# Performance work log

Hardware: AMD Instinct MI355X
Metric: run time of the kernel (lower is better)

## Reference

```python
import jax, jax.numpy as jnp
import numpy as np

N = 50000      # nodes
E = 800000     # edges (avg degree 16)
D = 64         # emb_dim
L = 5          # num_layer
BN_EPS = 1e-5


def setup_inputs() -> dict:
    key = jax.random.key(0)
    ks = jax.random.split(key, 10)
    x = jax.random.randint(ks[0], (N,), 0, 1)                      # indices into 1-row embedding
    edge_index = jax.random.randint(ks[1], (2, E), 0, N)
    edge_attr = jax.random.normal(ks[2], (E, 7), dtype=jnp.float32)
    s = lambda k, shape: (jax.random.normal(k, shape, dtype=jnp.float32) * 0.05)
    node_emb = s(ks[3], (1, D))
    # per-layer GINConv params, stacked on a leading layer axis for lax.scan
    We = s(ks[4], (L, 7, D));   be = jnp.zeros((L, D), jnp.float32)      # edge_encoder
    eps = jnp.zeros((L,), jnp.float32)                                   # GIN eps
    W1 = s(ks[5], (L, D, 2 * D)); b1 = jnp.zeros((L, 2 * D), jnp.float32)  # mlp linear1
    g1 = jnp.ones((L, 2 * D), jnp.float32); bb1 = jnp.zeros((L, 2 * D), jnp.float32)  # mlp BN
    W2 = s(ks[6], (L, 2 * D, D)); b2 = jnp.zeros((L, D), jnp.float32)    # mlp linear2
    g2 = jnp.ones((L, D), jnp.float32); bb2 = jnp.zeros((L, D), jnp.float32)  # outer BN
    return dict(x=x, edge_index=edge_index, edge_attr=edge_attr, node_emb=node_emb,
                We=We, be=be, eps=eps, W1=W1, b1=b1, g1=g1, bb1=bb1,
                W2=W2, b2=b2, g2=g2, bb2=bb2)


def _bn(a, g, b):
    # BatchNorm1d in training mode: batch statistics over node axis, biased var
    m = a.mean(axis=0)
    v = jnp.var(a, axis=0)
    return (a - m) * jax.lax.rsqrt(v + BN_EPS) * g + b


def reference(x, edge_index, edge_attr, node_emb, We, be, eps,
              W1, b1, g1, bb1, W2, b2, g2, bb2):
    src, dst = edge_index[0], edge_index[1]
    h = node_emb[x]                                    # [N, D]
    relu_flags = jnp.arange(L) < (L - 1)               # ReLU on all but last layer

    def step(h, p):
        We_, be_, eps_, W1_, b1_, g1_, bb1_, W2_, b2_, g2_, bb2_, flag = p
        ee = edge_attr @ We_ + be_                     # [E, D] edge embeddings
        msg = jax.nn.relu(h[src] + ee)                 # gather + elementwise
        agg = jax.ops.segment_sum(msg, dst, num_segments=N)  # scatter-add
        z = (1.0 + eps_) * h + agg                     # GIN combine
        a = jax.nn.relu(_bn(z @ W1_ + b1_, g1_, bb1_)) # mlp: lin -> BN -> ReLU
        hb = _bn(a @ W2_ + b2_, g2_, bb2_)             # lin -> outer BN
        h_new = jnp.where(flag, jax.nn.relu(hb), hb)   # dropout omitted (eval)
        return h_new, None

    h, _ = jax.lax.scan(step, h, (We, be, eps, W1, b1, g1, bb1, W2, b2, g2, bb2, relu_flags))
    return h                                           # JK='last'
```

## Files before the change

### kernel.cpp

```cpp
#include <hip/hip_runtime.h>
#include <hip/hip_fp16.h>

#define NN 50000
#define EE 800000
#define NB 782
#define NBKT 196
#define BCAP 4608

typedef _Float16 f16x8 __attribute__((ext_vector_type(8)));
typedef _Float16 f16x2 __attribute__((ext_vector_type(2)));
typedef float f32x4 __attribute__((ext_vector_type(4)));

__device__ __forceinline__ unsigned h2u(__half2 h) {
    union { __half2 h; unsigned u; } c; c.h = h; return c.u;
}
__device__ __forceinline__ f16x2 u2h(unsigned u) {
    union { unsigned u; f16x2 h; } c; c.u = u; return c.h;
}

__global__ __launch_bounds__(256) void bin_kernel(
    const int* __restrict__ ei, const float* __restrict__ ea,
    int* __restrict__ bktcur, int4* __restrict__ srec,
    unsigned short* __restrict__ sdst)
{
    __shared__ int cnt[NBKT], base[NBKT];
    const int t = threadIdx.x;
    if (t < NBKT) cnt[t] = 0;
    __syncthreads();
    const int e0 = blockIdx.x << 12;
    int meta[16];
#pragma unroll
    for (int j = 0; j < 16; ++j) {
        const int e = e0 + (j << 8) + t;
        if (e < EE) {
            const int d = ei[EE + e];
            const int bk = d >> 8;
            const int rk = atomicAdd(&cnt[bk], 1);
            meta[j] = (rk << 16) | (bk << 8) | (d & 255);
        } else meta[j] = -1;
    }
    __syncthreads();
    if (t < NBKT) base[t] = cnt[t] ? atomicAdd(&bktcur[t], cnt[t]) : 0;
    __syncthreads();
#pragma unroll
    for (int j = 0; j < 16; ++j) {
        if (meta[j] < 0) continue;
        const int bk = (meta[j] >> 8) & 255;
        const int slot = base[bk] + (meta[j] >> 16);
        if (slot >= BCAP) continue;
        const int pos = bk * BCAP + slot;
        const int e = e0 + (j << 8) + t;
        const int src = ei[e];
        const float* a = ea + e * 7;
        const unsigned h0 = __half_as_ushort(__float2half(a[0]));
        const unsigned h1 = __half_as_ushort(__float2half(a[1]));
        const unsigned h2 = __half_as_ushort(__float2half(a[2]));
        const unsigned h3 = __half_as_ushort(__float2half(a[3]));
        const unsigned h4 = __half_as_ushort(__float2half(a[4]));
        const unsigned h5 = __half_as_ushort(__float2half(a[5]));
        const unsigned h6 = __half_as_ushort(__float2half(a[6]));
        srec[pos] = make_int4((int)(h0 | (h1 << 16)), (int)(h2 | (h3 << 16)),
                              (int)(h4 | (h5 << 16)), (int)(h6 | ((unsigned)src << 16)));
        sdst[pos] = (unsigned short)(meta[j] & 255);
    }
}

__global__ __launch_bounds__(256) void bcountA_kernel(
    const int* __restrict__ bktcur, const unsigned short* __restrict__ sdst,
    int* __restrict__ deg, int* __restrict__ bsum)
{
    __shared__ int nc[256], sm[256];
    const int b = blockIdx.x, t = threadIdx.x;
    nc[t] = 0;
    __syncthreads();
    const int nE = min(bktcur[b], BCAP);
    const int sb = b * BCAP;
    for (int i = t; i < nE; i += 256) atomicAdd(&nc[(int)sdst[sb + i]], 1);
    __syncthreads();
    const int node = (b << 8) + t;
    if (node < NN) deg[node] = nc[t];
    sm[t] = (node < NN) ? ((nc[t] + 7) & ~7) : 0;
    __syncthreads();
    for (int o = 128; o > 0; o >>= 1) {
        if (t < o) sm[t] += sm[t + o];
        __syncthreads();
    }
    if (t == 0) bsum[b] = sm[0];
}

__global__ __launch_bounds__(256) void scanB_kernel(int* __restrict__ bsum) {
    __shared__ int sm[256];
    const int t = threadIdx.x;
    const int v = (t < 196) ? bsum[t] : 0;
    sm[t] = v;
    __syncthreads();
    for (int o = 1; o < 256; o <<= 1) {
        const int u = (t >= o) ? sm[t - o] : 0;
        __syncthreads();
        sm[t] += u;
        __syncthreads();
    }
    bsum[t] = sm[t] - v;
}

__global__ __launch_bounds__(256) void scanC_kernel(const int* __restrict__ deg,
                                                    const int* __restrict__ bsum,
                                                    int* __restrict__ off) {
    __shared__ int sm[256];
    const int t = threadIdx.x;
    const int i = (blockIdx.x << 8) + t;
    const int v = (i < NN) ? ((deg[i] + 7) & ~7) : 0;
    sm[t] = v;
    __syncthreads();
    for (int o = 1; o < 256; o <<= 1) {
        const int u = (t >= o) ? sm[t - o] : 0;
        __syncthreads();
        sm[t] += u;
        __syncthreads();
    }
    const int excl = bsum[blockIdx.x] + sm[t] - v;
    if (i < NN) off[i] = excl;
    else if (i == NN) off[NN] = excl;
}

__global__ __launch_bounds__(256) void place2_kernel(
    const int* __restrict__ bktcur, const int* __restrict__ off,
    const int4* __restrict__ srec, const unsigned short* __restrict__ sdst,
    int4* __restrict__ pea)
{
    __shared__ int curs[256];
    const int b = blockIdx.x, t = threadIdx.x;
    const int node = (b << 8) + t;
    curs[t] = (node < NN) ? off[node] : 0;
    __syncthreads();
    const int nE = min(bktcur[b], BCAP);
    const int sb = b * BCAP;
    for (int i = t; i < nE; i += 256) {
        const int ln = (int)sdst[sb + i];
        const int p = atomicAdd(&curs[ln], 1);
        pea[p] = srec[sb + i];
    }
    __syncthreads();
    if (node < NN) {
        const int end = off[node + 1];
        for (int p = curs[t]; p < end; ++p)
            pea[p] = make_int4(0, 0, 0, (int)(((unsigned)NN) << 16));
    }
}

__global__ __launch_bounds__(256) void wprep_kernel(
    const float* __restrict__ W1, const float* __restrict__ W2,
    const float* __restrict__ We, const float* __restrict__ be,
    _Float16* __restrict__ W1s, _Float16* __restrict__ W2s,
    unsigned* __restrict__ Wepk, unsigned* __restrict__ be2)
{
    const int i = (blockIdx.x << 8) + threadIdx.x;
    if (i < 40960) {
        const int l = i >> 13, j = i & 8191, k = j >> 7, n = j & 127;
        W1s[(l << 13) + ((((k >> 3) << 7) + n) << 3) + (k & 7)] = (_Float16)W1[i];
    } else if (i < 81920) {
        const int i2 = i - 40960;
        const int l = i2 >> 13, j = i2 & 8191, k = j >> 6, n = j & 63;
        W2s[(l << 13) + ((((k >> 3) << 6) + n) << 3) + (k & 7)] = (_Float16)W2[i2];
    } else if (i < 83040) {
        const int i3 = i - 81920;
        const int l = i3 / 224;
        const int r = i3 - l * 224;
        const int k = r >> 5, s = r & 31;
        const float* W = We + l * 448 + (k << 6) + (s << 1);
        Wepk[i3] = h2u(__floats2half2_rn(W[0], W[1]));
    } else if (i < 83200) {
        const int i4 = i - 83040;
        const int l = i4 >> 5, s = i4 & 31;
        const float* B = be + (l << 6) + (s << 1);
        be2[i4] = h2u(__floats2half2_rn(B[0], B[1]));
    }
}

__global__ __launch_bounds__(256) void hprep_kernel(
    const float* __restrict__ y2, const float* __restrict__ acc2,
    const float* __restrict__ g2p, const float* __restrict__ bb2p,
    __half* __restrict__ h16)
{
    __shared__ float scshL[128];
    const int t = threadIdx.x;
    if (t < 64) {
        float ss = 0.f, qq = 0.f;
#pragma unroll
        for (int c = 0; c < 8; ++c) {
            ss += acc2[(c << 7) + t];
            qq += acc2[(c << 7) + 64 + t];
        }
        const float m = ss * (1.0f / NN);
        const float v = fmaxf(qq * (1.0f / NN) - m * m, 0.0f);
        const float sc = g2p[t] * rsqrtf(v + 1e-5f);
        scshL[t] = sc;
        scshL[64 + t] = bb2p[t] - m * sc;
    }
    __syncthreads();
    const int i4 = (blockIdx.x << 8) + t;
    const float4 v = ((const float4*)y2)[i4];
    const int d0 = (i4 << 2) & 63;
    const float a = fmaxf(fmaf(v.x, scshL[d0 + 0], scshL[64 + d0 + 0]), 0.f);
    const float b = fmaxf(fmaf(v.y, scshL[d0 + 1], scshL[64 + d0 + 1]), 0.f);
    const float c = fmaxf(fmaf(v.z, scshL[d0 + 2], scshL[64 + d0 + 2]), 0.f);
    const float d = fmaxf(fmaf(v.w, scshL[d0 + 3], scshL[64 + d0 + 3]), 0.f);
    *(int2*)(h16 + (i4 << 2)) =
        make_int2((int)h2u(__floats2half2_rn(a, b)),
                  (int)h2u(__floats2half2_rn(c, d)));
}

__global__ __launch_bounds__(256) void hprep0_kernel(
    const int* __restrict__ x, const float* __restrict__ nemb,
    __half* __restrict__ h16, unsigned* __restrict__ z32)
{
    const int i4 = (blockIdx.x << 8) + threadIdx.x;
    if (blockIdx.x == 0 && threadIdx.x < 32)
        ((unsigned*)h16)[(NN << 5) + threadIdx.x] = 0xFBFFFBFFu;
    if (i4 < 1536) z32[1600000 + i4] = 0u;
    const int n = i4 >> 4;
    const float4 v = ((const float4*)nemb)[(x[n] << 4) + (i4 & 15)];
    *(int2*)(h16 + (i4 << 2)) =
        make_int2((int)h2u(__floats2half2_rn(v.x, v.y)),
                  (int)h2u(__floats2half2_rn(v.z, v.w)));
}

__global__ __launch_bounds__(256) void gather_kernel(
    const int* __restrict__ off, const int4* __restrict__ pea,
    const unsigned* __restrict__ h32,
    const unsigned* __restrict__ Wepk, const unsigned* __restrict__ be2,
    const float* __restrict__ epsp,
    unsigned* __restrict__ z32)
{
    const int t = threadIdx.x;
    const int lane = t & 63;
    const int s = lane & 31;
    const int n = (blockIdx.x << 3) + ((t >> 6) << 1) + (lane >> 5);

    const f16x2 w0 = u2h(Wepk[s]),       w1 = u2h(Wepk[32 + s]),
                w2 = u2h(Wepk[64 + s]),  w3 = u2h(Wepk[96 + s]),
                w4 = u2h(Wepk[128 + s]), w5 = u2h(Wepk[160 + s]),
                w6 = u2h(Wepk[192 + s]);
    const f16x2 beh = u2h(be2[s]);

    const int e0 = off[n], e1 = off[n + 1];

    f16x2 acc2 = (f16x2){(_Float16)0.f, (_Float16)0.f};
    int e = e0;
    if (((e1 - e0) >> 3) & 1) {
        int4 pk[8];
#pragma unroll
        for (int j = 0; j < 8; ++j) pk[j] = pea[e + j];
        unsigned hv[8];
#pragma unroll
        for (int j = 0; j < 8; ++j)
            hv[j] = h32[(((int)(((unsigned)pk[j].w) >> 16)) << 5) + s];
#pragma unroll
        for (int j = 0; j < 8; ++j) {
            const f16x2 a01 = u2h((unsigned)pk[j].x);
            const f16x2 a23 = u2h((unsigned)pk[j].y);
            const f16x2 a45 = u2h((unsigned)pk[j].z);
            const f16x2 a6x = u2h((unsigned)pk[j].w);
            f16x2 ee = beh;
            ee += (f16x2){a01[0], a01[0]} * w0;
            ee += (f16x2){a01[1], a01[1]} * w1;
            ee += (f16x2){a23[0], a23[0]} * w2;
            ee += (f16x2){a23[1], a23[1]} * w3;
            ee += (f16x2){a45[0], a45[0]} * w4;
            ee += (f16x2){a45[1], a45[1]} * w5;
            ee += (f16x2){a6x[0], a6x[0]} * w6;
            f16x2 m2 = u2h(hv[j]) + ee;
            const _Float16 zz = (_Float16)0.f;
            m2 = (f16x2){ m2[0] > zz ? m2[0] : zz, m2[1] > zz ? m2[1] : zz };
            acc2 += m2;
        }
        e += 8;
    }
    for (; e < e1; e += 16) {
        int4 pk[16];
#pragma unroll
        for (int j = 0; j < 16; ++j) pk[j] = pea[e + j];
        unsigned hv[16];
#pragma unroll
        for (int j = 0; j < 16; ++j)
            hv[j] = h32[(((int)(((unsigned)pk[j].w) >> 16)) << 5) + s];
#pragma unroll
        for (int j = 0; j < 16; ++j) {
            const f16x2 a01 = u2h((unsigned)pk[j].x);
            const f16x2 a23 = u2h((unsigned)pk[j].y);
            const f16x2 a45 = u2h((unsigned)pk[j].z);
            const f16x2 a6x = u2h((unsigned)pk[j].w);
            f16x2 ee = beh;
            ee += (f16x2){a01[0], a01[0]} * w0;
            ee += (f16x2){a01[1], a01[1]} * w1;
            ee += (f16x2){a23[0], a23[0]} * w2;
            ee += (f16x2){a23[1], a23[1]} * w3;
            ee += (f16x2){a45[0], a45[0]} * w4;
            ee += (f16x2){a45[1], a45[1]} * w5;
            ee += (f16x2){a6x[0], a6x[0]} * w6;
            f16x2 m2 = u2h(hv[j]) + ee;
            const _Float16 zz = (_Float16)0.f;
            m2 = (f16x2){ m2[0] > zz ? m2[0] : zz, m2[1] > zz ? m2[1] : zz };
            acc2 += m2;
        }
    }
    const f16x2 hn2 = u2h(h32[(n << 5) + s]);
    const float e1f = 1.0f + epsp[0];
    const float zLo = fmaf(e1f, (float)hn2[0], (float)acc2[0]);
    const float zHi = fmaf(e1f, (float)hn2[1], (float)acc2[1]);
    z32[(n << 5) + s] = h2u(__floats2half2_rn(zLo, zHi));
}

__global__ __launch_bounds__(256) void mm1_kernel(
    const _Float16* __restrict__ z16, const _Float16* __restrict__ W1s,
    const float* __restrict__ b1p, _Float16* __restrict__ y1h,
    float* __restrict__ acc1)
{
    __shared__ float smS[4][128], smQ[4][128];
    const int t = threadIdx.x;
    const int wv = t >> 6, lane = t & 63;
    const int q = lane >> 4, ln = lane & 15;
    const int r0 = blockIdx.x << 6;

    const int rowm = r0 + (wv << 4) + ln;
    const f16x8 af0 = *(const f16x8*)(z16 + rowm * 64 + (q << 3));
    const f16x8 af1 = *(const f16x8*)(z16 + rowm * 64 + 32 + (q << 3));

    f32x4 acc[8];
#pragma unroll
    for (int n0 = 0; n0 < 8; ++n0) acc[n0] = (f32x4){0.f, 0.f, 0.f, 0.f};
#pragma unroll
    for (int n0 = 0; n0 < 8; ++n0) {
        const f16x8 bf0 = *(const f16x8*)(W1s + (((q << 7) + (n0 << 4) + ln) << 3));
        const f16x8 bf1 = *(const f16x8*)(W1s + ((((4 + q) << 7) + (n0 << 4) + ln) << 3));
        acc[n0] = __builtin_amdgcn_mfma_f32_16x16x32_f16(af0, bf0, acc[n0], 0, 0, 0);
        acc[n0] = __builtin_amdgcn_mfma_f32_16x16x32_f16(af1, bf1, acc[n0], 0, 0, 0);
    }

    const int baseRow = r0 + (wv << 4) + (q << 2);
#pragma unroll
    for (int n0 = 0; n0 < 8; ++n0) {
        const int col = (n0 << 4) + ln;
        const float bb = b1p[col];
        float s = 0.f, sq = 0.f;
#pragma unroll
        for (int rg = 0; rg < 4; ++rg) {
            const int row = baseRow + rg;
            const float y = acc[n0][rg] + bb;
            y1h[row * 128 + col] = (_Float16)y;
            const float m = (row < NN) ? 1.f : 0.f;
            s = fmaf(m, y, s); sq = fmaf(m, y * y, sq);
        }
        s += __shfl_xor(s, 16); s += __shfl_xor(s, 32);
        sq += __shfl_xor(sq, 16); sq += __shfl_xor(sq, 32);
        if (lane < 16) { smS[wv][col] = s; smQ[wv][col] = sq; }
    }
    __syncthreads();
    if (t < 128) {
        const float s4 = smS[0][t] + smS[1][t] + smS[2][t] + smS[3][t];
        const float q4 = smQ[0][t] + smQ[1][t] + smQ[2][t] + smQ[3][t];
        float* a1 = acc1 + ((blockIdx.x & 7) << 8);
        atomicAdd(&a1[t], s4);
        atomicAdd(&a1[128 + t], q4);
    }
}

__global__ __launch_bounds__(256) void mm2_kernel(
    const _Float16* __restrict__ y1h, const float* __restrict__ acc1,
    const float* __restrict__ g1p, const float* __restrict__ bb1p,
    const _Float16* __restrict__ W2s, const float* __restrict__ b2,
    float* __restrict__ y2, float* __restrict__ acc2)
{
    __shared__ float smS[4][64], smQ[4][64];
    __shared__ float scshL[256];
    const int t = threadIdx.x;
    const int wv = t >> 6, lane = t & 63;
    const int q = lane >> 4, ln = lane & 15;
    const int r0 = blockIdx.x << 6;

    if (t < 128) {
        float ss = 0.f, qq = 0.f;
#pragma unroll
        for (int c = 0; c < 8; ++c) {
            ss += acc1[(c << 8) + t];
            qq += acc1[(c << 8) + 128 + t];
        }
        const float m = ss * (1.0f / NN);
        const float v = fmaxf(qq * (1.0f / NN) - m * m, 0.0f);
        const float sc = g1p[t] * rsqrtf(v + 1e-5f);
        scshL[t] = sc;
        scshL[128 + t] = bb1p[t] - m * sc;
    }
    __syncthreads();

    const int rowm = r0 + (wv << 4) + ln;
    f16x8 af[4];
#pragma unroll
    for (int ks = 0; ks < 4; ++ks) {
        const int k0 = (ks << 5) + (q << 3);
        const f16x8 raw = *(const f16x8*)(y1h + rowm * 128 + k0);
        f16x8 a;
#pragma unroll
        for (int j = 0; j < 8; ++j) {
            const float sc = scshL[k0 + j], sh = scshL[128 + k0 + j];
            a[j] = (_Float16)fmaxf(fmaf((float)raw[j], sc, sh), 0.f);
        }
        af[ks] = a;
    }

    f32x4 acc[4];
#pragma unroll
    for (int n0 = 0; n0 < 4; ++n0) acc[n0] = (f32x4){0.f, 0.f, 0.f, 0.f};
#pragma unroll
    for (int n0 = 0; n0 < 4; ++n0) {
#pragma unroll
        for (int ks = 0; ks < 4; ++ks) {
            const f16x8 bf = *(const f16x8*)(
                W2s + (((((ks << 2) + q) << 6) + (n0 << 4) + ln) << 3));
            acc[n0] = __builtin_amdgcn_mfma_f32_16x16x32_f16(af[ks], bf, acc[n0], 0, 0, 0);
        }
    }

    const int baseRow = r0 + (wv << 4) + (q << 2);
#pragma unroll
    for (int n0 = 0; n0 < 4; ++n0) {
        const int col = (n0 << 4) + ln;
        const float bb = b2[col];
        float s = 0.f, sq = 0.f;
#pragma unroll
        for (int rg = 0; rg < 4; ++rg) {
            const int row = baseRow + rg;
            const float y = acc[n0][rg] + bb;
            y2[row * 64 + col] = y;
            const float m = (row < NN) ? 1.f : 0.f;
            s = fmaf(m, y, s); sq = fmaf(m, y * y, sq);
        }
        s += __shfl_xor(s, 16); s += __shfl_xor(s, 32);
        sq += __shfl_xor(sq, 16); sq += __shfl_xor(sq, 32);
        if (lane < 16) { smS[wv][col] = s; smQ[wv][col] = sq; }
    }
    __syncthreads();
    if (t < 64) {
        const float s4 = smS[0][t] + smS[1][t] + smS[2][t] + smS[3][t];
        const float q4 = smQ[0][t] + smQ[1][t] + smQ[2][t] + smQ[3][t];
        float* a2 = acc2 + ((blockIdx.x & 7) << 7);
        atomicAdd(&a2[t], s4);
        atomicAdd(&a2[64 + t], q4);
    }
}

__global__ __launch_bounds__(256) void final_kernel(
    const float* __restrict__ y2, const float* __restrict__ acc2,
    const float* __restrict__ g2p, const float* __restrict__ bb2p,
    float* __restrict__ out)
{
    __shared__ float scshL[128];
    const int t = threadIdx.x;
    if (t < 64) {
        float ss = 0.f, qq = 0.f;
#pragma unroll
        for (int c = 0; c < 8; ++c) {
            ss += acc2[(c << 7) + t];
            qq += acc2[(c << 7) + 64 + t];
        }
        const float m = ss * (1.0f / NN);
        const float v = fmaxf(qq * (1.0f / NN) - m * m, 0.0f);
        const float sc = g2p[t] * rsqrtf(v + 1e-5f);
        scshL[t] = sc;
        scshL[64 + t] = bb2p[t] - m * sc;
    }
    __syncthreads();
    const int i4 = (blockIdx.x << 8) + t;
    const float4 v = ((const float4*)y2)[i4];
    const int d0 = (i4 << 2) & 63;
    float4 o;
    o.x = fmaf(v.x, scshL[d0 + 0], scshL[64 + d0 + 0]);
    o.y = fmaf(v.y, scshL[d0 + 1], scshL[64 + d0 + 1]);
    o.z = fmaf(v.z, scshL[d0 + 2], scshL[64 + d0 + 2]);
    o.w = fmaf(v.w, scshL[d0 + 3], scshL[64 + d0 + 3]);
    ((float4*)out)[i4] = o;
}

extern "C" void kernel_launch(void* const* d_in, const int* in_sizes, int n_in,
                              void* d_out, int out_size, void* d_ws, size_t ws_size,
                              hipStream_t stream)
{
    const int*   x    = (const int*)d_in[0];
    const int*   ei   = (const int*)d_in[1];
    const float* ea   = (const float*)d_in[2];
    const float* nemb = (const float*)d_in[3];
    const float* We   = (const float*)d_in[4];
    const float* be   = (const float*)d_in[5];
    const float* eps  = (const float*)d_in[6];
    const float* W1   = (const float*)d_in[7];
    const float* b1   = (const float*)d_in[8];
    const float* g1   = (const float*)d_in[9];
    const float* bb1  = (const float*)d_in[10];
    const float* W2   = (const float*)d_in[11];
    const float* b2   = (const float*)d_in[12];
    const float* g2   = (const float*)d_in[13];
    const float* bb2  = (const float*)d_in[14];
    float* out = (float*)d_out;

    int*      iws   = (int*)d_ws;
    float*    fws   = (float*)d_ws;
    int*      off   = iws + 0;
    int*      deg   = iws + 50048;
    int*      bsum  = iws + 150144;
    int*      bktcur= iws + 150784;
    float*    accbuf= fws + 151040;
    _Float16* W1s   = (_Float16*)(fws + 451072);
    _Float16* W2s   = (_Float16*)(fws + 471552);
    unsigned* Wepk  = (unsigned*)(fws + 492032);
    unsigned* be2   = (unsigned*)(fws + 493152);
    int4*     pea   = (int4*)(iws + 493312);
    _Float16* z16   = (_Float16*)(fws + 5093312);
    _Float16* y1h   = (_Float16*)(fws + 6694848);
    float*    y2    = fws + 6694848;
    __half*   h16   = (__half*)(fws + 9897920);

    int4*           srec = (int4*)(fws + 5093312);
    unsigned short* sdst = (unsigned short*)(fws + 9897920);

    hipMemsetAsync(bktcur, 0, (166400 - 150784) * sizeof(int), stream);

    bin_kernel    <<<196,  256, 0, stream>>>(ei, ea, bktcur, srec, sdst);
    bcountA_kernel<<<NBKT, 256, 0, stream>>>(bktcur, sdst, deg, bsum);
    scanB_kernel  <<<1,    256, 0, stream>>>(bsum);
    scanC_kernel  <<<196,  256, 0, stream>>>(deg, bsum, off);
    place2_kernel <<<NBKT, 256, 0, stream>>>(bktcur, off, srec, sdst, pea);
    wprep_kernel  <<<325,  256, 0, stream>>>(W1, W2, We, be, W1s, W2s, Wepk, be2);
    hprep0_kernel <<<3125, 256, 0, stream>>>(x, nemb, h16, (unsigned*)z16);

    for (int l = 0; l < 5; ++l) {
        float* acc1 = accbuf + l * 3072;
        float* acc2 = accbuf + l * 3072 + 2048;

        gather_kernel<<<6250, 256, 0, stream>>>(
            off, pea, (const unsigned*)h16, Wepk + l * 224, be2 + l * 32,
            eps + l, (unsigned*)z16);

        mm1_kernel<<<NB, 256, 0, stream>>>(z16, W1s + l * 8192, b1 + l * 128,
                                           y1h, acc1);

        mm2_kernel<<<NB, 256, 0, stream>>>(y1h, acc1, g1 + l * 128, bb1 + l * 128,
                                           W2s + l * 8192, b2 + l * 64, y2, acc2);

        if (l < 4)
            hprep_kernel<<<3125, 256, 0, stream>>>(y2, acc2, g2 + l * 64,
                                                   bb2 + l * 64, h16);
    }

    final_kernel<<<3125, 256, 0, stream>>>(y2, accbuf + 4 * 3072 + 2048,
                                           g2 + 4 * 64, bb2 + 4 * 64, out);
}
```

Measured before the change: 417.5 us.

## Fuse CSR build into per-bucket kernel with fixed slots and merge prep kernels

Replaces the count/scan/scan/place chain with one kernel per bucket. Each bucket computes a local prefix sum and writes its edges into a fixed-capacity slot region, and start/end pairs replace the global offset array. The weight-prep and initial-h kernels are merged into one launch. This removes four launches and the global scan passes, but adds padding gaps in the edge array and assumes each bucket's padded edge count fits its fixed slot.

```diff
diff --git a/kernel.cpp b/kernel.cpp
--- a/kernel.cpp
+++ b/kernel.cpp
@@ -6,6 +6,7 @@
 #define NB 782
 #define NBKT 196
 #define BCAP 4608
+#define PSLOT 6144
 
 typedef _Float16 f16x8 __attribute__((ext_vector_type(8)));
 typedef _Float16 f16x2 __attribute__((ext_vector_type(2)));
@@ -65,11 +66,12 @@
     }
 }
 
-__global__ __launch_bounds__(256) void bcountA_kernel(
-    const int* __restrict__ bktcur, const unsigned short* __restrict__ sdst,
-    int* __restrict__ deg, int* __restrict__ bsum)
-{
-    __shared__ int nc[256], sm[256];
+__global__ __launch_bounds__(256) void buildB_kernel(
+    const int* __restrict__ bktcur, const int4* __restrict__ srec,
+    const unsigned short* __restrict__ sdst,
+    int2* __restrict__ offSE, int4* __restrict__ pea)
+{
+    __shared__ int nc[256], sm[256], curs[256];
     const int b = blockIdx.x, t = threadIdx.x;
     nc[t] = 0;
     __syncthreads();
@@ -78,21 +80,9 @@
     for (int i = t; i < nE; i += 256) atomicAdd(&nc[(int)sdst[sb + i]], 1);
     __syncthreads();
     const int node = (b << 8) + t;
-    if (node < NN) deg[node] = nc[t];
-    sm[t] = (node < NN) ? ((nc[t] + 7) & ~7) : 0;
-    __syncthreads();
-    for (int o = 128; o > 0; o >>= 1) {
-        if (t < o) sm[t] += sm[t + o];
-        __syncthreads();
-    }
-    if (t == 0) bsum[b] = sm[0];
-}
-
-__global__ __launch_bounds__(256) void scanB_kernel(int* __restrict__ bsum) {
-    __shared__ int sm[256];
-    const int t = threadIdx.x;
-    const int v = (t < 196) ? bsum[t] : 0;
-    sm[t] = v;
+    const int used = nc[t];
+    const int pd = (node < NN) ? ((used + 7) & ~7) : 0;
+    sm[t] = pd;
     __syncthreads();
     for (int o = 1; o < 256; o <<= 1) {
         const int u = (t >= o) ? sm[t - o] : 0;
@@ -100,41 +90,10 @@
         sm[t] += u;
         __syncthreads();
     }
-    bsum[t] = sm[t] - v;
-}
-
-__global__ __launch_bounds__(256) void scanC_kernel(const int* __restrict__ deg,
-                                                    const int* __restrict__ bsum,
-                                                    int* __restrict__ off) {
-    __shared__ int sm[256];
-    const int t = threadIdx.x;
-    const int i = (blockIdx.x << 8) + t;
-    const int v = (i < NN) ? ((deg[i] + 7) & ~7) : 0;
-    sm[t] = v;
-    __syncthreads();
-    for (int o = 1; o < 256; o <<= 1) {
-        const int u = (t >= o) ? sm[t - o] : 0;
-        __syncthreads();
-        sm[t] += u;
-        __syncthreads();
-    }
-    const int excl = bsum[blockIdx.x] + sm[t] - v;
-    if (i < NN) off[i] = excl;
-    else if (i == NN) off[NN] = excl;
-}
-
-__global__ __launch_bounds__(256) void place2_kernel(
-    const int* __restrict__ bktcur, const int* __restrict__ off,
-    const int4* __restrict__ srec, const unsigned short* __restrict__ sdst,
-    int4* __restrict__ pea)
-{
-    __shared__ int curs[256];
-    const int b = blockIdx.x, t = threadIdx.x;
-    const int node = (b << 8) + t;
-    curs[t] = (node < NN) ? off[node] : 0;
-    __syncthreads();
-    const int nE = min(bktcur[b], BCAP);
-    const int sb = b * BCAP;
+    const int st = b * PSLOT + sm[t] - pd;
+    if (node < NN) offSE[node] = make_int2(st, st + pd);
+    curs[t] = st;
+    __syncthreads();
     for (int i = t; i < nE; i += 256) {
         const int ln = (int)sdst[sb + i];
         const int p = atomicAdd(&curs[ln], 1);
@@ -142,19 +101,33 @@
     }
     __syncthreads();
     if (node < NN) {
-        const int end = off[node + 1];
+        const int end = st + pd;
         for (int p = curs[t]; p < end; ++p)
             pea[p] = make_int4(0, 0, 0, (int)(((unsigned)NN) << 16));
     }
 }
 
-__global__ __launch_bounds__(256) void wprep_kernel(
+__global__ __launch_bounds__(256) void prep_kernel(
+    const int* __restrict__ x, const float* __restrict__ nemb,
+    __half* __restrict__ h16, unsigned* __restrict__ z32,
     const float* __restrict__ W1, const float* __restrict__ W2,
     const float* __restrict__ We, const float* __restrict__ be,
     _Float16* __restrict__ W1s, _Float16* __restrict__ W2s,
     unsigned* __restrict__ Wepk, unsigned* __restrict__ be2)
 {
-    const int i = (blockIdx.x << 8) + threadIdx.x;
+    if (blockIdx.x < 3125) {
+        const int i4 = (blockIdx.x << 8) + threadIdx.x;
+        if (blockIdx.x == 0 && threadIdx.x < 32)
+            ((unsigned*)h16)[(NN << 5) + threadIdx.x] = 0xFBFFFBFFu;
+        if (i4 < 1536) z32[1600000 + i4] = 0u;
+        const int n = i4 >> 4;
+        const float4 v = ((const float4*)nemb)[(x[n] << 4) + (i4 & 15)];
+        *(int2*)(h16 + (i4 << 2)) =
+            make_int2((int)h2u(__floats2half2_rn(v.x, v.y)),
+                      (int)h2u(__floats2half2_rn(v.z, v.w)));
+        return;
+    }
+    const int i = ((blockIdx.x - 3125) << 8) + threadIdx.x;
     if (i < 40960) {
         const int l = i >> 13, j = i & 8191, k = j >> 7, n = j & 127;
         W1s[(l << 13) + ((((k >> 3) << 7) + n) << 3) + (k & 7)] = (_Float16)W1[i];
@@ -210,23 +183,8 @@
                   (int)h2u(__floats2half2_rn(c, d)));
 }
 
-__global__ __launch_bounds__(256) void hprep0_kernel(
-    const int* __restrict__ x, const float* __restrict__ nemb,
-    __half* __restrict__ h16, unsigned* __restrict__ z32)
-{
-    const int i4 = (blockIdx.x << 8) + threadIdx.x;
-    if (blockIdx.x == 0 && threadIdx.x < 32)
-        ((unsigned*)h16)[(NN << 5) + threadIdx.x] = 0xFBFFFBFFu;
-    if (i4 < 1536) z32[1600000 + i4] = 0u;
-    const int n = i4 >> 4;
-    const float4 v = ((const float4*)nemb)[(x[n] << 4) + (i4 & 15)];
-    *(int2*)(h16 + (i4 << 2)) =
-        make_int2((int)h2u(__floats2half2_rn(v.x, v.y)),
-                  (int)h2u(__floats2half2_rn(v.z, v.w)));
-}
-
 __global__ __launch_bounds__(256) void gather_kernel(
-    const int* __restrict__ off, const int4* __restrict__ pea,
+    const int2* __restrict__ offSE, const int4* __restrict__ pea,
     const unsigned* __restrict__ h32,
     const unsigned* __restrict__ Wepk, const unsigned* __restrict__ be2,
     const float* __restrict__ epsp,
@@ -243,7 +201,8 @@
                 w6 = u2h(Wepk[192 + s]);
     const f16x2 beh = u2h(be2[s]);
 
-    const int e0 = off[n], e1 = off[n + 1];
+    const int2 se = offSE[n];
+    const int e0 = se.x, e1 = se.y;
 
     f16x2 acc2 = (f16x2){(_Float16)0.f, (_Float16)0.f};
     int e = e0;
@@ -426,18 +385,18 @@
     for (int n0 = 0; n0 < 4; ++n0) {
         const int col = (n0 << 4) + ln;
         const float bb = b2[col];
-        float s = 0.f, sq = 0.f;
+        float sa = 0.f, sq = 0.f;
 #pragma unroll
         for (int rg = 0; rg < 4; ++rg) {
             const int row = baseRow + rg;
             const float y = acc[n0][rg] + bb;
             y2[row * 64 + col] = y;
             const float m = (row < NN) ? 1.f : 0.f;
-            s = fmaf(m, y, s); sq = fmaf(m, y * y, sq);
-        }
-        s += __shfl_xor(s, 16); s += __shfl_xor(s, 32);
+            sa = fmaf(m, y, sa); sq = fmaf(m, y * y, sq);
+        }
+        sa += __shfl_xor(sa, 16); sa += __shfl_xor(sa, 32);
         sq += __shfl_xor(sq, 16); sq += __shfl_xor(sq, 32);
-        if (lane < 16) { smS[wv][col] = s; smQ[wv][col] = sq; }
+        if (lane < 16) { smS[wv][col] = sa; smQ[wv][col] = sq; }
     }
     __syncthreads();
     if (t < 64) {
@@ -504,40 +463,35 @@
 
     int*      iws   = (int*)d_ws;
     float*    fws   = (float*)d_ws;
-    int*      off   = iws + 0;
-    int*      deg   = iws + 50048;
-    int*      bsum  = iws + 150144;
-    int*      bktcur= iws + 150784;
-    float*    accbuf= fws + 151040;
-    _Float16* W1s   = (_Float16*)(fws + 451072);
-    _Float16* W2s   = (_Float16*)(fws + 471552);
-    unsigned* Wepk  = (unsigned*)(fws + 492032);
-    unsigned* be2   = (unsigned*)(fws + 493152);
-    int4*     pea   = (int4*)(iws + 493312);
-    _Float16* z16   = (_Float16*)(fws + 5093312);
-    _Float16* y1h   = (_Float16*)(fws + 6694848);
-    float*    y2    = fws + 6694848;
-    __half*   h16   = (__half*)(fws + 9897920);
-
-    int4*           srec = (int4*)(fws + 5093312);
-    unsigned short* sdst = (unsigned short*)(fws + 9897920);
-
-    hipMemsetAsync(bktcur, 0, (166400 - 150784) * sizeof(int), stream);
-
-    bin_kernel    <<<196,  256, 0, stream>>>(ei, ea, bktcur, srec, sdst);
-    bcountA_kernel<<<NBKT, 256, 0, stream>>>(bktcur, sdst, deg, bsum);
-    scanB_kernel  <<<1,    256, 0, stream>>>(bsum);
-    scanC_kernel  <<<196,  256, 0, stream>>>(deg, bsum, off);
-    place2_kernel <<<NBKT, 256, 0, stream>>>(bktcur, off, srec, sdst, pea);
-    wprep_kernel  <<<325,  256, 0, stream>>>(W1, W2, We, be, W1s, W2s, Wepk, be2);
-    hprep0_kernel <<<3125, 256, 0, stream>>>(x, nemb, h16, (unsigned*)z16);
+    int2*     offSE = (int2*)iws;
+    int*      bktcur= iws + 100096;
+    float*    accbuf= fws + 100352;
+    _Float16* W1s   = (_Float16*)(fws + 115712);
+    _Float16* W2s   = (_Float16*)(fws + 136192);
+    unsigned* Wepk  = (unsigned*)(fws + 156672);
+    unsigned* be2   = (unsigned*)(fws + 157792);
+    int4*     pea   = (int4*)(iws + 157952);
+    _Float16* z16   = (_Float16*)(fws + 4974848);
+    _Float16* y1h   = (_Float16*)(fws + 6576384);
+    float*    y2    = fws + 6576384;
+    __half*   h16   = (__half*)(fws + 9779456);
+
+    int4*           srec = (int4*)(fws + 4974848);
+    unsigned short* sdst = (unsigned short*)(fws + 9779456);
+
+    hipMemsetAsync(bktcur, 0, (115712 - 100096) * sizeof(int), stream);
+
+    bin_kernel   <<<196,  256, 0, stream>>>(ei, ea, bktcur, srec, sdst);
+    buildB_kernel<<<NBKT, 256, 0, stream>>>(bktcur, srec, sdst, offSE, pea);
+    prep_kernel  <<<3450, 256, 0, stream>>>(x, nemb, h16, (unsigned*)z16,
+                                            W1, W2, We, be, W1s, W2s, Wepk, be2);
 
     for (int l = 0; l < 5; ++l) {
         float* acc1 = accbuf + l * 3072;
         float* acc2 = accbuf + l * 3072 + 2048;
 
         gather_kernel<<<6250, 256, 0, stream>>>(
-            off, pea, (const unsigned*)h16, Wepk + l * 224, be2 + l * 32,
+            offSE, pea, (const unsigned*)h16, Wepk + l * 224, be2 + l * 32,
             eps + l, (unsigned*)z16);
 
         mm1_kernel<<<NB, 256, 0, stream>>>(z16, W1s + l * 8192, b1 + l * 128,
```

Measured after the change: 408.9 us. -2.1%, faster.
